# Performance work log

Measured on AMD Instinct MI355X. Metric: run time of the kernel, lower is better.

The kernel has to match this reference:

```python
import jax, jax.numpy as jnp
import numpy as np

B, S, D = 64, 1024, 64

def setup_inputs() -> dict:
    key = jax.random.key(0)
    kq, kk, kv, krk, krv = jax.random.split(key, 5)
    q = jax.random.normal(kq, (B, S, D), jnp.float32)
    k = jax.random.normal(kk, (B, S, D), jnp.float32)
    v = jax.random.normal(kv, (B, S, D), jnp.float32)
    # relative positional bias tables: R_k[q_pos, k_pos, d], R_v[q_pos, v_pos, d]
    R_k = jax.random.normal(krk, (S, S, D), jnp.float32) * 0.02
    R_v = jax.random.normal(krv, (S, S, D), jnp.float32) * 0.02
    mask = jnp.tril(jnp.ones((1, S, S), jnp.int32))  # causal mask
    return {"q": q, "k": k, "v": v, "R_k": R_k, "R_v": R_v, "mask": mask, "one_direction": 1}

def reference(q, k, v, R_k, R_v, mask, one_direction):
    d_k = k.shape[-1]
    # scores = q @ k^T + relative-key bias, THEN scaled (matches original op order)
    scores = jnp.matmul(q, jnp.swapaxes(k, -2, -1))
    scores = scores + jnp.einsum('bqd,qkd->bqk', q, R_k)
    scores = scores * jnp.asarray(1.0 / np.sqrt(d_k), scores.dtype)
    if one_direction:
        scores = jnp.where(mask == 0, jnp.asarray(-1e9, scores.dtype), scores)
    attn = jax.nn.softmax(scores, axis=-1)
    # output = attn @ v + relative-value bias  (dropout p=0.0 -> identity)
    out = jnp.matmul(attn, v) + jnp.einsum('bqv,qvd->bqd', attn, R_v)
    return (out, attn)
```

## Files before the change

### kernel.cpp

```cpp
#include <hip/hip_runtime.h>
#include <math.h>

namespace {

constexpr int S_ = 1024;
constexpr int B_ = 64;
constexpr int D_ = 64;
constexpr float SCALE = 0.125f;

__global__ __launch_bounds__(256) void bias_kernel(
    const float* __restrict__ q, const float* __restrict__ Rk,
    float* __restrict__ attn) {
  const int qp = (S_ - 1) - (int)blockIdx.y;
  const int chunk = blockIdx.x;
  if (chunk * 256 > qp) return;

  __shared__ float Qs[64][65];
  __shared__ float Rs[64][65];
  const int t = threadIdx.x;

  for (int i = 0; i < 16; ++i) {
    const int flat = t + i * 256;
    const int b = flat >> 6, d = flat & 63;
    Qs[b][d] = q[((b << 10) + qp) * 64 + d];
  }

  const int k0 = (t & 15) * 4;
  const int b0 = (t >> 4) * 4;

  for (int s = 0; s < 4; ++s) {
    const int kb = chunk * 256 + s * 64;
    if (kb > qp) break;
    __syncthreads();
    for (int i = 0; i < 4; ++i) {
      const int flat = t + i * 256;
      const int kk = flat >> 4, dd = (flat & 15) * 4;
      const float4 r4 = *(const float4*)(Rk + ((qp << 10) + kb + kk) * 64 + dd);
      Rs[kk][dd + 0] = r4.x; Rs[kk][dd + 1] = r4.y;
      Rs[kk][dd + 2] = r4.z; Rs[kk][dd + 3] = r4.w;
    }
    __syncthreads();

    float acc[4][4];
    #pragma unroll
    for (int i = 0; i < 4; ++i)
      #pragma unroll
      for (int j = 0; j < 4; ++j) acc[i][j] = 0.f;

    for (int d = 0; d < 64; ++d) {
      float rk[4], qv[4];
      #pragma unroll
      for (int i = 0; i < 4; ++i) rk[i] = Rs[k0 + i][d];
      #pragma unroll
      for (int j = 0; j < 4; ++j) qv[j] = Qs[b0 + j][d];
      #pragma unroll
      for (int i = 0; i < 4; ++i)
        #pragma unroll
        for (int j = 0; j < 4; ++j) acc[i][j] += rk[i] * qv[j];
    }

    #pragma unroll
    for (int j = 0; j < 4; ++j) {
      const int b = b0 + j;
      float* row = attn + (((b << 10) + qp) << 10) + kb + k0;
      if (kb + k0 + 3 <= qp) {
        *(float4*)row = make_float4(acc[0][j], acc[1][j], acc[2][j], acc[3][j]);
      } else {
        for (int i = 0; i < 4; ++i)
          if (kb + k0 + i <= qp) row[i] = acc[i][j];
      }
    }
  }
}

__global__ __launch_bounds__(256) void attn_kernel(
    const float* __restrict__ qg, const float* __restrict__ kg,
    const float* __restrict__ vg, float* attn, float* __restrict__ outg) {
  const int b = blockIdx.y;
  const int qti = 15 - (int)blockIdx.x;
  const int qb = qti * 64;

  __shared__ float Qs[64][65];
  __shared__ float KVs[64][65];
  __shared__ float Ps[64][65];
  __shared__ float redm[64][16];
  __shared__ float redl[64][16];

  const int t = threadIdx.x;
  const int k0 = (t & 15) * 4;
  const int q0 = (t >> 4) * 4;
  const int d0 = k0;

  for (int i = 0; i < 16; ++i) {
    const int flat = t + i * 256;
    const int qq = flat >> 6, d = flat & 63;
    Qs[qq][d] = qg[((b << 10) + qb + qq) * 64 + d];
  }

  float m[4], l[4];
  #pragma unroll
  for (int j = 0; j < 4; ++j) { m[j] = -INFINITY; l[j] = 0.f; }

  const int ntiles = qti + 1;

  for (int tt = 0; tt < ntiles; ++tt) {
    const int kb = tt * 64;
    __syncthreads();
    for (int i = 0; i < 4; ++i) {
      const int flat = t + i * 256;
      const int kk = flat >> 4, dd = (flat & 15) * 4;
      const float4 r4 = *(const float4*)(kg + ((b << 10) + kb + kk) * 64 + dd);
      KVs[kk][dd + 0] = r4.x; KVs[kk][dd + 1] = r4.y;
      KVs[kk][dd + 2] = r4.z; KVs[kk][dd + 3] = r4.w;
    }
    __syncthreads();

    float acc[4][4];
    #pragma unroll
    for (int j = 0; j < 4; ++j)
      #pragma unroll
      for (int i = 0; i < 4; ++i) acc[j][i] = 0.f;
    for (int d = 0; d < 64; ++d) {
      float kv[4], qv[4];
      #pragma unroll
      for (int i = 0; i < 4; ++i) kv[i] = KVs[k0 + i][d];
      #pragma unroll
      for (int j = 0; j < 4; ++j) qv[j] = Qs[q0 + j][d];
      #pragma unroll
      for (int j = 0; j < 4; ++j)
        #pragma unroll
        for (int i = 0; i < 4; ++i) acc[j][i] += qv[j] * kv[i];
    }

    #pragma unroll
    for (int j = 0; j < 4; ++j) {
      const int qq = qb + q0 + j;
      const float4 b4 = *(const float4*)(attn + (((b << 10) + qq) << 10) + kb + k0);
      const float barr[4] = {b4.x, b4.y, b4.z, b4.w};
      float sv[4];
      float tmax = -INFINITY;
      #pragma unroll
      for (int i = 0; i < 4; ++i) {
        sv[i] = (acc[j][i] + barr[i]) * SCALE;
        if (kb + k0 + i <= qq) tmax = fmaxf(tmax, sv[i]);
      }
      if (tmax > -INFINITY) {
        const float mnew = fmaxf(m[j], tmax);
        float ladd = 0.f;
        #pragma unroll
        for (int i = 0; i < 4; ++i)
          if (kb + k0 + i <= qq) ladd += __expf(sv[i] - mnew);
        l[j] = l[j] * __expf(m[j] - mnew) + ladd;
        m[j] = mnew;
      }
    }
  }

  __syncthreads();
  #pragma unroll
  for (int j = 0; j < 4; ++j) {
    redm[q0 + j][t & 15] = m[j];
    redl[q0 + j][t & 15] = l[j];
  }
  __syncthreads();
  float mf[4], linv[4];
  #pragma unroll
  for (int j = 0; j < 4; ++j) {
    float mm = -INFINITY;
    for (int i = 0; i < 16; ++i) mm = fmaxf(mm, redm[q0 + j][i]);
    float ll = 0.f;
    for (int i = 0; i < 16; ++i) ll += redl[q0 + j][i] * __expf(redm[q0 + j][i] - mm);
    mf[j] = mm;
    linv[j] = 1.f / ll;
  }

  float accpv[4][4];
  #pragma unroll
  for (int j = 0; j < 4; ++j)
    #pragma unroll
    for (int i = 0; i < 4; ++i) accpv[j][i] = 0.f;

  for (int tt = 0; tt < ntiles; ++tt) {
    const int kb = tt * 64;
    __syncthreads();
    for (int i = 0; i < 4; ++i) {
      const int flat = t + i * 256;
      const int kk = flat >> 4, dd = (flat & 15) * 4;
      const float4 r4 = *(const float4*)(kg + ((b << 10) + kb + kk) * 64 + dd);
      KVs[kk][dd + 0] = r4.x; KVs[kk][dd + 1] = r4.y;
      KVs[kk][dd + 2] = r4.z; KVs[kk][dd + 3] = r4.w;
    }
    __syncthreads();

    float acc[4][4];
    #pragma unroll
    for (int j = 0; j < 4; ++j)
      #pragma unroll
      for (int i = 0; i < 4; ++i) acc[j][i] = 0.f;
    for (int d = 0; d < 64; ++d) {
      float kv[4], qv[4];
      #pragma unroll
      for (int i = 0; i < 4; ++i) kv[i] = KVs[k0 + i][d];
      #pragma unroll
      for (int j = 0; j < 4; ++j) qv[j] = Qs[q0 + j][d];
      #pragma unroll
      for (int j = 0; j < 4; ++j)
        #pragma unroll
        for (int i = 0; i < 4; ++i) acc[j][i] += qv[j] * kv[i];
    }

    #pragma unroll
    for (int j = 0; j < 4; ++j) {
      const int qq = qb + q0 + j;
      float* arow = attn + (((b << 10) + qq) << 10) + kb + k0;
      const float4 b4 = *(const float4*)arow;
      const float barr[4] = {b4.x, b4.y, b4.z, b4.w};
      float p[4];
      #pragma unroll
      for (int i = 0; i < 4; ++i) {
        const float s = (acc[j][i] + barr[i]) * SCALE;
        p[i] = (kb + k0 + i <= qq) ? __expf(s - mf[j]) * linv[j] : 0.f;
      }
      *(float4*)arow = make_float4(p[0], p[1], p[2], p[3]);
      #pragma unroll
      for (int i = 0; i < 4; ++i) Ps[q0 + j][k0 + i] = p[i];
    }
    __syncthreads();
    for (int i = 0; i < 4; ++i) {
      const int flat = t + i * 256;
      const int kk = flat >> 4, dd = (flat & 15) * 4;
      const float4 r4 = *(const float4*)(vg + ((b << 10) + kb + kk) * 64 + dd);
      KVs[kk][dd + 0] = r4.x; KVs[kk][dd + 1] = r4.y;
      KVs[kk][dd + 2] = r4.z; KVs[kk][dd + 3] = r4.w;
    }
    __syncthreads();
    for (int kk = 0; kk < 64; ++kk) {
      float pv[4], vv[4];
      #pragma unroll
      for (int j = 0; j < 4; ++j) pv[j] = Ps[q0 + j][kk];
      #pragma unroll
      for (int i = 0; i < 4; ++i) vv[i] = KVs[kk][d0 + i];
      #pragma unroll
      for (int j = 0; j < 4; ++j)
        #pragma unroll
        for (int i = 0; i < 4; ++i) accpv[j][i] += pv[j] * vv[i];
    }
  }

  for (int kb = ntiles * 64; kb < S_; kb += 64) {
    #pragma unroll
    for (int j = 0; j < 4; ++j) {
      const int qq = qb + q0 + j;
      *(float4*)(attn + (((b << 10) + qq) << 10) + kb + k0) =
          make_float4(0.f, 0.f, 0.f, 0.f);
    }
  }

  #pragma unroll
  for (int j = 0; j < 4; ++j) {
    const int qq = qb + q0 + j;
    *(float4*)(outg + ((b << 10) + qq) * 64 + d0) =
        make_float4(accpv[j][0], accpv[j][1], accpv[j][2], accpv[j][3]);
  }
}

__global__ __launch_bounds__(256) void rvout_kernel(
    const float* __restrict__ Rv, const float* __restrict__ attn,
    float* outg) {
  const int qp = (S_ - 1) - (int)blockIdx.x;
  __shared__ float As[64][65];
  __shared__ float Rs[64][65];
  const int t = threadIdx.x;
  const int d0 = (t & 15) * 4;
  const int b0 = (t >> 4) * 4;

  float acc[4][4];
  #pragma unroll
  for (int j = 0; j < 4; ++j)
    #pragma unroll
    for (int i = 0; i < 4; ++i) acc[j][i] = 0.f;

  const int ntiles = (qp >> 6) + 1;
  for (int tt = 0; tt < ntiles; ++tt) {
    const int kb = tt * 64;
    __syncthreads();
    for (int i = 0; i < 4; ++i) {
      const int flat = t + i * 256;
      const int r = flat >> 4, c4 = (flat & 15) * 4;
      const float4 a4 = *(const float4*)(attn + (((r << 10) + qp) << 10) + kb + c4);
      As[r][c4 + 0] = a4.x; As[r][c4 + 1] = a4.y;
      As[r][c4 + 2] = a4.z; As[r][c4 + 3] = a4.w;
      const float4 r4 = *(const float4*)(Rv + ((qp << 10) + kb + r) * 64 + c4);
      Rs[r][c4 + 0] = r4.x; Rs[r][c4 + 1] = r4.y;
      Rs[r][c4 + 2] = r4.z; Rs[r][c4 + 3] = r4.w;
    }
    __syncthreads();
    for (int kk = 0; kk < 64; ++kk) {
      float av[4], rv[4];
      #pragma unroll
      for (int j = 0; j < 4; ++j) av[j] = As[b0 + j][kk];
      #pragma unroll
      for (int i = 0; i < 4; ++i) rv[i] = Rs[kk][d0 + i];
      #pragma unroll
      for (int j = 0; j < 4; ++j)
        #pragma unroll
        for (int i = 0; i < 4; ++i) acc[j][i] += av[j] * rv[i];
    }
  }

  #pragma unroll
  for (int j = 0; j < 4; ++j) {
    float* po = outg + (((b0 + j) << 10) + qp) * 64 + d0;
    float4 o = *(const float4*)po;
    o.x += acc[j][0]; o.y += acc[j][1]; o.z += acc[j][2]; o.w += acc[j][3];
    *(float4*)po = o;
  }
}

}

extern "C" void kernel_launch(void* const* d_in, const int* in_sizes, int n_in,
                              void* d_out, int out_size, void* d_ws, size_t ws_size,
                              hipStream_t stream) {
  const float* q  = (const float*)d_in[0];
  const float* k  = (const float*)d_in[1];
  const float* v  = (const float*)d_in[2];
  const float* Rk = (const float*)d_in[3];
  const float* Rv = (const float*)d_in[4];

  float* out  = (float*)d_out;
  float* attn = out + (size_t)B_ * S_ * D_;

  hipLaunchKernelGGL(bias_kernel, dim3(4, S_), dim3(256), 0, stream, q, Rk, attn);
  hipLaunchKernelGGL(attn_kernel, dim3(16, B_), dim3(256), 0, stream, q, k, v, attn, out);
  hipLaunchKernelGGL(rvout_kernel, dim3(S_), dim3(256), 0, stream, Rv, attn, out);
}
```

Measured before the change: 1.306 ms.

## Port bias, attention and Rv kernels to bf16 MFMA with swizzled LDS

Replaces the scalar FP32 outer-product loops in all three kernels with 16x16x32 bf16 MFMA instructions. Operands are converted to bf16 on load into XOR-swizzled shared memory. QK^T keeps near-FP32 accuracy through a hi/lo split that costs three MFMAs per tile. Row max and row sum reductions move from a shared-memory reduction to wavefront shuffles. The kernels are bound by reading the large R_k/R_v tables and the attn matrix from memory, so the compute speedup may matter less than it appears, and the bf16 rounding of R_k, R_v, P and V loosens accuracy.

```diff
diff --git a/kernel.cpp b/kernel.cpp
--- a/kernel.cpp
+++ b/kernel.cpp
@@ -7,6 +7,22 @@
 constexpr int B_ = 64;
 constexpr int D_ = 64;
 constexpr float SCALE = 0.125f;
+
+typedef __attribute__((ext_vector_type(8))) short bf16x8;
+typedef __attribute__((ext_vector_type(4))) float f32x4;
+
+__device__ __forceinline__ ushort f2bf(float x) {
+  union { float f; uint u; } c; c.f = x;
+  return (ushort)((c.u + 0x7fffu + ((c.u >> 16) & 1u)) >> 16);
+}
+__device__ __forceinline__ float bf2f(ushort h) {
+  union { uint u; float f; } c; c.u = ((uint)h) << 16;
+  return c.f;
+}
+
+#define SWZ(row, c) (((row) << 6) + ((c) ^ (((row) & 7) << 3)))
+
+#define MFMA(a, b, c) __builtin_amdgcn_mfma_f32_16x16x32_bf16((a), (b), (c), 0, 0, 0)
 
 __global__ __launch_bounds__(256) void bias_kernel(
     const float* __restrict__ q, const float* __restrict__ Rk,
@@ -15,60 +31,56 @@
   const int chunk = blockIdx.x;
   if (chunk * 256 > qp) return;
 
-  __shared__ float Qs[64][65];
-  __shared__ float Rs[64][65];
+  __shared__ __align__(16) ushort Rh[64 * 64];
+
   const int t = threadIdx.x;
-
-  for (int i = 0; i < 16; ++i) {
-    const int flat = t + i * 256;
-    const int b = flat >> 6, d = flat & 63;
-    Qs[b][d] = q[((b << 10) + qp) * 64 + d];
-  }
-
-  const int k0 = (t & 15) * 4;
-  const int b0 = (t >> 4) * 4;
-
-  for (int s = 0; s < 4; ++s) {
-    const int kb = chunk * 256 + s * 64;
+  const int wid = t >> 6, lane = t & 63;
+  const int llo = lane & 15, lhi = lane >> 4;
+  const f32x4 fz = {0.f, 0.f, 0.f, 0.f};
+
+  bf16x8 qa[2];
+  {
+    const int brow = wid * 16 + llo;
+    const float* qp_ = q + (((brow << 10) + qp) << 6) + lhi * 8;
+    #pragma unroll
+    for (int s = 0; s < 2; ++s)
+      #pragma unroll
+      for (int j = 0; j < 8; ++j) qa[s][j] = (short)f2bf(qp_[s * 32 + j]);
+  }
+
+  for (int s4 = 0; s4 < 4; ++s4) {
+    const int kb = chunk * 256 + s4 * 64;
     if (kb > qp) break;
     __syncthreads();
+    #pragma unroll
     for (int i = 0; i < 4; ++i) {
       const int flat = t + i * 256;
       const int kk = flat >> 4, dd = (flat & 15) * 4;
-      const float4 r4 = *(const float4*)(Rk + ((qp << 10) + kb + kk) * 64 + dd);
-      Rs[kk][dd + 0] = r4.x; Rs[kk][dd + 1] = r4.y;
-      Rs[kk][dd + 2] = r4.z; Rs[kk][dd + 3] = r4.w;
-    }
-    __syncthreads();
-
-    float acc[4][4];
-    #pragma unroll
-    for (int i = 0; i < 4; ++i)
-      #pragma unroll
-      for (int j = 0; j < 4; ++j) acc[i][j] = 0.f;
-
-    for (int d = 0; d < 64; ++d) {
-      float rk[4], qv[4];
-      #pragma unroll
-      for (int i = 0; i < 4; ++i) rk[i] = Rs[k0 + i][d];
-      #pragma unroll
-      for (int j = 0; j < 4; ++j) qv[j] = Qs[b0 + j][d];
-      #pragma unroll
-      for (int i = 0; i < 4; ++i)
-        #pragma unroll
-        for (int j = 0; j < 4; ++j) acc[i][j] += rk[i] * qv[j];
-    }
-
-    #pragma unroll
-    for (int j = 0; j < 4; ++j) {
-      const int b = b0 + j;
-      float* row = attn + (((b << 10) + qp) << 10) + kb + k0;
-      if (kb + k0 + 3 <= qp) {
-        *(float4*)row = make_float4(acc[0][j], acc[1][j], acc[2][j], acc[3][j]);
-      } else {
-        for (int i = 0; i < 4; ++i)
-          if (kb + k0 + i <= qp) row[i] = acc[i][j];
-      }
+      const float4 r4 = *(const float4*)(Rk + (((qp << 10) + kb + kk) << 6) + dd);
+      *(ushort4*)&Rh[SWZ(kk, dd)] =
+          make_ushort4(f2bf(r4.x), f2bf(r4.y), f2bf(r4.z), f2bf(r4.w));
+    }
+    __syncthreads();
+
+    f32x4 acc[4];
+    #pragma unroll
+    for (int kt = 0; kt < 4; ++kt) acc[kt] = fz;
+    #pragma unroll
+    for (int s = 0; s < 2; ++s)
+      #pragma unroll
+      for (int kt = 0; kt < 4; ++kt) {
+        const bf16x8 rb =
+            *(const bf16x8*)&Rh[SWZ(kt * 16 + llo, s * 32 + lhi * 8)];
+        acc[kt] = MFMA(qa[s], rb, acc[kt]);
+      }
+
+    #pragma unroll
+    for (int r = 0; r < 4; ++r) {
+      const int bb = wid * 16 + lhi * 4 + r;
+      float* row = attn + (((bb << 10) + qp) << 10) + kb + llo;
+      #pragma unroll
+      for (int kt = 0; kt < 4; ++kt)
+        if (kb + kt * 16 + llo <= qp) row[kt * 16] = acc[kt][r];
     }
   }
 }
@@ -79,188 +91,202 @@
   const int b = blockIdx.y;
   const int qti = 15 - (int)blockIdx.x;
   const int qb = qti * 64;
-
-  __shared__ float Qs[64][65];
-  __shared__ float KVs[64][65];
-  __shared__ float Ps[64][65];
-  __shared__ float redm[64][16];
-  __shared__ float redl[64][16];
+  const int ntiles = qti + 1;
+
+  __shared__ __align__(16) ushort Khi[64 * 64];
+  __shared__ __align__(16) ushort Klo[64 * 64];
+  __shared__ __align__(16) ushort VT[64 * 64];
+  __shared__ __align__(16) ushort Pl[4 * 16 * 64];
 
   const int t = threadIdx.x;
-  const int k0 = (t & 15) * 4;
-  const int q0 = (t >> 4) * 4;
-  const int d0 = k0;
-
-  for (int i = 0; i < 16; ++i) {
-    const int flat = t + i * 256;
-    const int qq = flat >> 6, d = flat & 63;
-    Qs[qq][d] = qg[((b << 10) + qb + qq) * 64 + d];
+  const int wid = t >> 6, lane = t & 63;
+  const int llo = lane & 15, lhi = lane >> 4;
+  const f32x4 fz = {0.f, 0.f, 0.f, 0.f};
+
+  bf16x8 qh[2], ql[2];
+  {
+    const int qrow = qb + wid * 16 + llo;
+    const float* qp_ = qg + (((b << 10) + qrow) << 6) + lhi * 8;
+    #pragma unroll
+    for (int s = 0; s < 2; ++s)
+      #pragma unroll
+      for (int j = 0; j < 8; ++j) {
+        const float x = qp_[s * 32 + j];
+        const ushort h = f2bf(x);
+        qh[s][j] = (short)h;
+        ql[s][j] = (short)f2bf(x - bf2f(h));
+      }
   }
 
   float m[4], l[4];
   #pragma unroll
-  for (int j = 0; j < 4; ++j) { m[j] = -INFINITY; l[j] = 0.f; }
-
-  const int ntiles = qti + 1;
+  for (int r = 0; r < 4; ++r) { m[r] = -INFINITY; l[r] = 0.f; }
 
   for (int tt = 0; tt < ntiles; ++tt) {
     const int kb = tt * 64;
     __syncthreads();
+    #pragma unroll
     for (int i = 0; i < 4; ++i) {
       const int flat = t + i * 256;
       const int kk = flat >> 4, dd = (flat & 15) * 4;
-      const float4 r4 = *(const float4*)(kg + ((b << 10) + kb + kk) * 64 + dd);
-      KVs[kk][dd + 0] = r4.x; KVs[kk][dd + 1] = r4.y;
-      KVs[kk][dd + 2] = r4.z; KVs[kk][dd + 3] = r4.w;
-    }
-    __syncthreads();
-
-    float acc[4][4];
-    #pragma unroll
-    for (int j = 0; j < 4; ++j)
-      #pragma unroll
-      for (int i = 0; i < 4; ++i) acc[j][i] = 0.f;
-    for (int d = 0; d < 64; ++d) {
-      float kv[4], qv[4];
-      #pragma unroll
-      for (int i = 0; i < 4; ++i) kv[i] = KVs[k0 + i][d];
-      #pragma unroll
-      for (int j = 0; j < 4; ++j) qv[j] = Qs[q0 + j][d];
-      #pragma unroll
-      for (int j = 0; j < 4; ++j)
-        #pragma unroll
-        for (int i = 0; i < 4; ++i) acc[j][i] += qv[j] * kv[i];
-    }
-
-    #pragma unroll
-    for (int j = 0; j < 4; ++j) {
-      const int qq = qb + q0 + j;
-      const float4 b4 = *(const float4*)(attn + (((b << 10) + qq) << 10) + kb + k0);
-      const float barr[4] = {b4.x, b4.y, b4.z, b4.w};
+      const float4 r4 = *(const float4*)(kg + (((b << 10) + kb + kk) << 6) + dd);
+      const ushort h0 = f2bf(r4.x), h1 = f2bf(r4.y);
+      const ushort h2 = f2bf(r4.z), h3 = f2bf(r4.w);
+      const int idx = SWZ(kk, dd);
+      *(ushort4*)&Khi[idx] = make_ushort4(h0, h1, h2, h3);
+      *(ushort4*)&Klo[idx] = make_ushort4(
+          f2bf(r4.x - bf2f(h0)), f2bf(r4.y - bf2f(h1)),
+          f2bf(r4.z - bf2f(h2)), f2bf(r4.w - bf2f(h3)));
+    }
+    __syncthreads();
+
+    f32x4 acc[4];
+    #pragma unroll
+    for (int kt = 0; kt < 4; ++kt) acc[kt] = fz;
+    #pragma unroll
+    for (int s = 0; s < 2; ++s)
+      #pragma unroll
+      for (int kt = 0; kt < 4; ++kt) {
+        const int o = SWZ(kt * 16 + llo, s * 32 + lhi * 8);
+        const bf16x8 kh = *(const bf16x8*)&Khi[o];
+        const bf16x8 kl = *(const bf16x8*)&Klo[o];
+        acc[kt] = MFMA(qh[s], kh, acc[kt]);
+        acc[kt] = MFMA(ql[s], kh, acc[kt]);
+        acc[kt] = MFMA(qh[s], kl, acc[kt]);
+      }
+
+    #pragma unroll
+    for (int r = 0; r < 4; ++r) {
+      const int qq = qb + wid * 16 + lhi * 4 + r;
+      const float* bp = attn + (((b << 10) + qq) << 10) + kb + llo;
       float sv[4];
       float tmax = -INFINITY;
       #pragma unroll
-      for (int i = 0; i < 4; ++i) {
-        sv[i] = (acc[j][i] + barr[i]) * SCALE;
-        if (kb + k0 + i <= qq) tmax = fmaxf(tmax, sv[i]);
-      }
-      if (tmax > -INFINITY) {
-        const float mnew = fmaxf(m[j], tmax);
-        float ladd = 0.f;
-        #pragma unroll
-        for (int i = 0; i < 4; ++i)
-          if (kb + k0 + i <= qq) ladd += __expf(sv[i] - mnew);
-        l[j] = l[j] * __expf(m[j] - mnew) + ladd;
-        m[j] = mnew;
-      }
-    }
-  }
-
-  __syncthreads();
-  #pragma unroll
-  for (int j = 0; j < 4; ++j) {
-    redm[q0 + j][t & 15] = m[j];
-    redl[q0 + j][t & 15] = l[j];
-  }
-  __syncthreads();
-  float mf[4], linv[4];
-  #pragma unroll
-  for (int j = 0; j < 4; ++j) {
-    float mm = -INFINITY;
-    for (int i = 0; i < 16; ++i) mm = fmaxf(mm, redm[q0 + j][i]);
-    float ll = 0.f;
-    for (int i = 0; i < 16; ++i) ll += redl[q0 + j][i] * __expf(redm[q0 + j][i] - mm);
-    mf[j] = mm;
-    linv[j] = 1.f / ll;
-  }
-
-  float accpv[4][4];
-  #pragma unroll
-  for (int j = 0; j < 4; ++j)
-    #pragma unroll
-    for (int i = 0; i < 4; ++i) accpv[j][i] = 0.f;
+      for (int kt = 0; kt < 4; ++kt) {
+        const float s = (acc[kt][r] + bp[kt * 16]) * SCALE;
+        sv[kt] = s;
+        if (kb + kt * 16 + llo <= qq) tmax = fmaxf(tmax, s);
+      }
+      tmax = fmaxf(tmax, __shfl_xor(tmax, 1));
+      tmax = fmaxf(tmax, __shfl_xor(tmax, 2));
+      tmax = fmaxf(tmax, __shfl_xor(tmax, 4));
+      tmax = fmaxf(tmax, __shfl_xor(tmax, 8));
+      const float mnew = fmaxf(m[r], tmax);
+      const float corr = __expf(m[r] - mnew);
+      float ladd = 0.f;
+      #pragma unroll
+      for (int kt = 0; kt < 4; ++kt)
+        if (kb + kt * 16 + llo <= qq) ladd += __expf(sv[kt] - mnew);
+      l[r] = l[r] * corr + ladd;
+      m[r] = mnew;
+    }
+  }
+
+  float linv[4];
+  #pragma unroll
+  for (int r = 0; r < 4; ++r) {
+    float ls = l[r];
+    ls += __shfl_xor(ls, 1);
+    ls += __shfl_xor(ls, 2);
+    ls += __shfl_xor(ls, 4);
+    ls += __shfl_xor(ls, 8);
+    linv[r] = 1.f / ls;
+  }
+
+  f32x4 oacc[4];
+  #pragma unroll
+  for (int nt = 0; nt < 4; ++nt) oacc[nt] = fz;
 
   for (int tt = 0; tt < ntiles; ++tt) {
     const int kb = tt * 64;
     __syncthreads();
+    #pragma unroll
     for (int i = 0; i < 4; ++i) {
       const int flat = t + i * 256;
       const int kk = flat >> 4, dd = (flat & 15) * 4;
-      const float4 r4 = *(const float4*)(kg + ((b << 10) + kb + kk) * 64 + dd);
-      KVs[kk][dd + 0] = r4.x; KVs[kk][dd + 1] = r4.y;
-      KVs[kk][dd + 2] = r4.z; KVs[kk][dd + 3] = r4.w;
-    }
-    __syncthreads();
-
-    float acc[4][4];
-    #pragma unroll
-    for (int j = 0; j < 4; ++j)
-      #pragma unroll
-      for (int i = 0; i < 4; ++i) acc[j][i] = 0.f;
-    for (int d = 0; d < 64; ++d) {
-      float kv[4], qv[4];
-      #pragma unroll
-      for (int i = 0; i < 4; ++i) kv[i] = KVs[k0 + i][d];
-      #pragma unroll
-      for (int j = 0; j < 4; ++j) qv[j] = Qs[q0 + j][d];
-      #pragma unroll
-      for (int j = 0; j < 4; ++j)
-        #pragma unroll
-        for (int i = 0; i < 4; ++i) acc[j][i] += qv[j] * kv[i];
-    }
-
-    #pragma unroll
-    for (int j = 0; j < 4; ++j) {
-      const int qq = qb + q0 + j;
-      float* arow = attn + (((b << 10) + qq) << 10) + kb + k0;
-      const float4 b4 = *(const float4*)arow;
-      const float barr[4] = {b4.x, b4.y, b4.z, b4.w};
-      float p[4];
-      #pragma unroll
-      for (int i = 0; i < 4; ++i) {
-        const float s = (acc[j][i] + barr[i]) * SCALE;
-        p[i] = (kb + k0 + i <= qq) ? __expf(s - mf[j]) * linv[j] : 0.f;
-      }
-      *(float4*)arow = make_float4(p[0], p[1], p[2], p[3]);
-      #pragma unroll
-      for (int i = 0; i < 4; ++i) Ps[q0 + j][k0 + i] = p[i];
-    }
-    __syncthreads();
-    for (int i = 0; i < 4; ++i) {
-      const int flat = t + i * 256;
-      const int kk = flat >> 4, dd = (flat & 15) * 4;
-      const float4 r4 = *(const float4*)(vg + ((b << 10) + kb + kk) * 64 + dd);
-      KVs[kk][dd + 0] = r4.x; KVs[kk][dd + 1] = r4.y;
-      KVs[kk][dd + 2] = r4.z; KVs[kk][dd + 3] = r4.w;
-    }
-    __syncthreads();
-    for (int kk = 0; kk < 64; ++kk) {
-      float pv[4], vv[4];
-      #pragma unroll
-      for (int j = 0; j < 4; ++j) pv[j] = Ps[q0 + j][kk];
-      #pragma unroll
-      for (int i = 0; i < 4; ++i) vv[i] = KVs[kk][d0 + i];
-      #pragma unroll
-      for (int j = 0; j < 4; ++j)
-        #pragma unroll
-        for (int i = 0; i < 4; ++i) accpv[j][i] += pv[j] * vv[i];
-    }
-  }
-
-  for (int kb = ntiles * 64; kb < S_; kb += 64) {
-    #pragma unroll
-    for (int j = 0; j < 4; ++j) {
-      const int qq = qb + q0 + j;
-      *(float4*)(attn + (((b << 10) + qq) << 10) + kb + k0) =
-          make_float4(0.f, 0.f, 0.f, 0.f);
-    }
-  }
-
-  #pragma unroll
-  for (int j = 0; j < 4; ++j) {
-    const int qq = qb + q0 + j;
-    *(float4*)(outg + ((b << 10) + qq) * 64 + d0) =
-        make_float4(accpv[j][0], accpv[j][1], accpv[j][2], accpv[j][3]);
+      const float4 r4 = *(const float4*)(kg + (((b << 10) + kb + kk) << 6) + dd);
+      const ushort h0 = f2bf(r4.x), h1 = f2bf(r4.y);
+      const ushort h2 = f2bf(r4.z), h3 = f2bf(r4.w);
+      const int idx = SWZ(kk, dd);
+      *(ushort4*)&Khi[idx] = make_ushort4(h0, h1, h2, h3);
+      *(ushort4*)&Klo[idx] = make_ushort4(
+          f2bf(r4.x - bf2f(h0)), f2bf(r4.y - bf2f(h1)),
+          f2bf(r4.z - bf2f(h2)), f2bf(r4.w - bf2f(h3)));
+    }
+    #pragma unroll
+    for (int i = 0; i < 4; ++i) {
+      const int kk = lane;
+      const int dd = (wid + i * 4) * 4;
+      const float4 r4 = *(const float4*)(vg + (((b << 10) + kb + kk) << 6) + dd);
+      VT[SWZ(dd + 0, kk)] = f2bf(r4.x);
+      VT[SWZ(dd + 1, kk)] = f2bf(r4.y);
+      VT[SWZ(dd + 2, kk)] = f2bf(r4.z);
+      VT[SWZ(dd + 3, kk)] = f2bf(r4.w);
+    }
+    __syncthreads();
+
+    f32x4 acc[4];
+    #pragma unroll
+    for (int kt = 0; kt < 4; ++kt) acc[kt] = fz;
+    #pragma unroll
+    for (int s = 0; s < 2; ++s)
+      #pragma unroll
+      for (int kt = 0; kt < 4; ++kt) {
+        const int o = SWZ(kt * 16 + llo, s * 32 + lhi * 8);
+        const bf16x8 kh = *(const bf16x8*)&Khi[o];
+        const bf16x8 kl = *(const bf16x8*)&Klo[o];
+        acc[kt] = MFMA(qh[s], kh, acc[kt]);
+        acc[kt] = MFMA(ql[s], kh, acc[kt]);
+        acc[kt] = MFMA(qh[s], kl, acc[kt]);
+      }
+
+    #pragma unroll
+    for (int r = 0; r < 4; ++r) {
+      const int qq = qb + wid * 16 + lhi * 4 + r;
+      float* arow = attn + (((b << 10) + qq) << 10) + kb + llo;
+      const int prow = lhi * 4 + r;
+      #pragma unroll
+      for (int kt = 0; kt < 4; ++kt) {
+        const float s = (acc[kt][r] + arow[kt * 16]) * SCALE;
+        const float p =
+            (kb + kt * 16 + llo <= qq) ? __expf(s - m[r]) * linv[r] : 0.f;
+        arow[kt * 16] = p;
+        Pl[(wid << 10) + SWZ(prow, kt * 16 + llo)] = f2bf(p);
+      }
+    }
+    __syncthreads();
+
+    #pragma unroll
+    for (int s = 0; s < 2; ++s) {
+      const bf16x8 pa =
+          *(const bf16x8*)&Pl[(wid << 10) + SWZ(llo, s * 32 + lhi * 8)];
+      #pragma unroll
+      for (int nt = 0; nt < 4; ++nt) {
+        const bf16x8 vb = *(const bf16x8*)&VT[SWZ(nt * 16 + llo, s * 32 + lhi * 8)];
+        oacc[nt] = MFMA(pa, vb, oacc[nt]);
+      }
+    }
+  }
+
+  {
+    const int k0 = (t & 15) * 4;
+    const int q0 = (t >> 4) * 4;
+    for (int kb = ntiles * 64; kb < S_; kb += 64) {
+      #pragma unroll
+      for (int j = 0; j < 4; ++j) {
+        const int qq = qb + q0 + j;
+        *(float4*)(attn + (((b << 10) + qq) << 10) + kb + k0) =
+            make_float4(0.f, 0.f, 0.f, 0.f);
+      }
+    }
+  }
+
+  #pragma unroll
+  for (int r = 0; r < 4; ++r) {
+    const int qq = qb + wid * 16 + lhi * 4 + r;
+    #pragma unroll
+    for (int nt = 0; nt < 4; ++nt)
+      outg[(((b << 10) + qq) << 6) + nt * 16 + llo] = oacc[nt][r];
   }
 }
 
@@ -268,52 +294,62 @@
     const float* __restrict__ Rv, const float* __restrict__ attn,
     float* outg) {
   const int qp = (S_ - 1) - (int)blockIdx.x;
-  __shared__ float As[64][65];
-  __shared__ float Rs[64][65];
+  __shared__ __align__(16) ushort Ah[64 * 64];
+  __shared__ __align__(16) ushort RvT[64 * 64];
+
   const int t = threadIdx.x;
-  const int d0 = (t & 15) * 4;
-  const int b0 = (t >> 4) * 4;
-
-  float acc[4][4];
-  #pragma unroll
-  for (int j = 0; j < 4; ++j)
-    #pragma unroll
-    for (int i = 0; i < 4; ++i) acc[j][i] = 0.f;
+  const int wid = t >> 6, lane = t & 63;
+  const int llo = lane & 15, lhi = lane >> 4;
+  const f32x4 fz = {0.f, 0.f, 0.f, 0.f};
+
+  f32x4 oacc[4];
+  #pragma unroll
+  for (int nt = 0; nt < 4; ++nt) oacc[nt] = fz;
 
   const int ntiles = (qp >> 6) + 1;
   for (int tt = 0; tt < ntiles; ++tt) {
     const int kb = tt * 64;
     __syncthreads();
+    #pragma unroll
     for (int i = 0; i < 4; ++i) {
       const int flat = t + i * 256;
-      const int r = flat >> 4, c4 = (flat & 15) * 4;
-      const float4 a4 = *(const float4*)(attn + (((r << 10) + qp) << 10) + kb + c4);
-      As[r][c4 + 0] = a4.x; As[r][c4 + 1] = a4.y;
-      As[r][c4 + 2] = a4.z; As[r][c4 + 3] = a4.w;
-      const float4 r4 = *(const float4*)(Rv + ((qp << 10) + kb + r) * 64 + c4);
-      Rs[r][c4 + 0] = r4.x; Rs[r][c4 + 1] = r4.y;
-      Rs[r][c4 + 2] = r4.z; Rs[r][c4 + 3] = r4.w;
-    }
-    __syncthreads();
-    for (int kk = 0; kk < 64; ++kk) {
-      float av[4], rv[4];
-      #pragma unroll
-      for (int j = 0; j < 4; ++j) av[j] = As[b0 + j][kk];
-      #pragma unroll
-      for (int i = 0; i < 4; ++i) rv[i] = Rs[kk][d0 + i];
-      #pragma unroll
-      for (int j = 0; j < 4; ++j)
-        #pragma unroll
-        for (int i = 0; i < 4; ++i) acc[j][i] += av[j] * rv[i];
-    }
-  }
-
-  #pragma unroll
-  for (int j = 0; j < 4; ++j) {
-    float* po = outg + (((b0 + j) << 10) + qp) * 64 + d0;
-    float4 o = *(const float4*)po;
-    o.x += acc[j][0]; o.y += acc[j][1]; o.z += acc[j][2]; o.w += acc[j][3];
-    *(float4*)po = o;
+      const int bb = flat >> 4, cc = (flat & 15) * 4;
+      const float4 a4 =
+          *(const float4*)(attn + (((bb << 10) + qp) << 10) + kb + cc);
+      *(ushort4*)&Ah[SWZ(bb, cc)] =
+          make_ushort4(f2bf(a4.x), f2bf(a4.y), f2bf(a4.z), f2bf(a4.w));
+    }
+    #pragma unroll
+    for (int i = 0; i < 4; ++i) {
+      const int kk = lane;
+      const int dd = (wid + i * 4) * 4;
+      const float4 r4 = *(const float4*)(Rv + (((qp << 10) + kb + kk) << 6) + dd);
+      RvT[SWZ(dd + 0, kk)] = f2bf(r4.x);
+      RvT[SWZ(dd + 1, kk)] = f2bf(r4.y);
+      RvT[SWZ(dd + 2, kk)] = f2bf(r4.z);
+      RvT[SWZ(dd + 3, kk)] = f2bf(r4.w);
+    }
+    __syncthreads();
+
+    #pragma unroll
+    for (int s = 0; s < 2; ++s) {
+      const bf16x8 aa =
+          *(const bf16x8*)&Ah[SWZ(wid * 16 + llo, s * 32 + lhi * 8)];
+      #pragma unroll
+      for (int nt = 0; nt < 4; ++nt) {
+        const bf16x8 rb =
+            *(const bf16x8*)&RvT[SWZ(nt * 16 + llo, s * 32 + lhi * 8)];
+        oacc[nt] = MFMA(aa, rb, oacc[nt]);
+      }
+    }
+  }
+
+  #pragma unroll
+  for (int r = 0; r < 4; ++r) {
+    const int bb = wid * 16 + lhi * 4 + r;
+    float* po = outg + (((bb << 10) + qp) << 6);
+    #pragma unroll
+    for (int nt = 0; nt < 4; ++nt) po[nt * 16 + llo] += oacc[nt][r];
   }
 }
 
```

New measurement: 1.130 ms. 1.16x faster.
